# Performance work log

Measured on AMD Instinct MI355X. Metric: run time of the kernel, lower is better.

Reference implementation:

```python
import math
import jax, jax.numpy as jnp
import numpy as np

EMB = 1024
NHEADS = 16
CTX = 2048
LN_EPS = 1e-5


def new_gelu(x):
    c = math.sqrt(2.0 / math.pi)
    return 0.5 * x * (1.0 + jnp.tanh(c * (x + 0.044715 * x * x * x)))


def layer_norm(x, g, b):
    mu = jnp.mean(x, axis=-1, keepdims=True)
    var = jnp.mean(jnp.square(x - mu), axis=-1, keepdims=True)
    return (x - mu) * jax.lax.rsqrt(var + LN_EPS) * g + b


def setup_inputs() -> dict:
    key = jax.random.key(0)
    ks = jax.random.split(key, 12)
    s = 0.02
    return {
        "x": jax.random.normal(ks[0], (2, 2048, EMB), dtype=jnp.float32),
        "ln1_g": jnp.ones((EMB,), jnp.float32),
        "ln1_b": jnp.zeros((EMB,), jnp.float32),
        "W_attn": jax.random.normal(ks[1], (EMB, 3 * EMB), jnp.float32) * s,
        "b_attn": jnp.zeros((3 * EMB,), jnp.float32),
        "W_attn_proj": jax.random.normal(ks[2], (EMB, EMB), jnp.float32) * s,
        "b_attn_proj": jnp.zeros((EMB,), jnp.float32),
        "ln2_g": jnp.ones((EMB,), jnp.float32),
        "ln2_b": jnp.zeros((EMB,), jnp.float32),
        "W_fc": jax.random.normal(ks[3], (EMB, 4 * EMB), jnp.float32) * s,
        "b_fc": jnp.zeros((4 * EMB,), jnp.float32),
        "W_mlp_proj": jax.random.normal(ks[4], (4 * EMB, EMB), jnp.float32) * s,
        "b_mlp_proj": jnp.zeros((EMB,), jnp.float32),
    }


def reference(x, ln1_g, ln1_b, W_attn, b_attn, W_attn_proj, b_attn_proj,
              ln2_g, ln2_b, W_fc, b_fc, W_mlp_proj, b_mlp_proj):
    B, S, E = x.shape
    hd = E // NHEADS

    # x = ln_1(x)
    x = layer_norm(x, ln1_g, ln1_b)

    # attention on normalized x
    qkv = x @ W_attn + b_attn                      # [B,S,3E]
    q, k, v = jnp.split(qkv, 3, axis=-1)
    q = q.reshape(B, S, NHEADS, hd).transpose(0, 2, 1, 3)  # [B,H,S,hd]
    k = k.reshape(B, S, NHEADS, hd).transpose(0, 2, 1, 3)
    v = v.reshape(B, S, NHEADS, hd).transpose(0, 2, 1, 3)

    attn = jnp.einsum("bhqd,bhkd->bhqk", q, k) * (1.0 / math.sqrt(hd))
    causal = jnp.tril(jnp.ones((S, S), dtype=bool))
    attn = jnp.where(causal[None, None], attn, -jnp.inf)
    attn = jax.nn.softmax(attn, axis=-1)
    out = jnp.einsum("bhqk,bhkd->bhqd", attn, v)   # [B,H,S,hd]
    out = out.transpose(0, 2, 1, 3).reshape(B, S, E)
    out = out @ W_attn_proj + b_attn_proj

    x = x + out

    # x = ln_2(x)
    x = layer_norm(x, ln2_g, ln2_b)

    # MLP on normalized x
    h = new_gelu(x @ W_fc + b_fc)
    h = h @ W_mlp_proj + b_mlp_proj
    return x + h
```

## Files before the change

### kernel.cpp

```cpp
#include <hip/hip_runtime.h>
#include <cstdint>

typedef __attribute__((ext_vector_type(8))) short bf16x8;
typedef __attribute__((ext_vector_type(4))) float f32x4;
typedef __attribute__((ext_vector_type(4))) unsigned short u16x4;
typedef unsigned short u16;

#define LOG2E 1.44269504088896340736f

__device__ __forceinline__ u16 f2bf(float f) {
  unsigned u = __builtin_bit_cast(unsigned, f);
  u += 0x7FFFu + ((u >> 16) & 1u);
  return (u16)(u >> 16);
}
__device__ __forceinline__ float bf2f(u16 h) {
  return __builtin_bit_cast(float, ((unsigned)h) << 16);
}

#define GLOAD_LDS16(g, l)                                                              \
  __builtin_amdgcn_global_load_lds((const __attribute__((address_space(1))) void*)(g), \
                                   (__attribute__((address_space(3))) void*)(l), 16, 0, 0)

__global__ __launch_bounds__(256) void k_transpose_bf16(
    const float* __restrict__ W, u16* __restrict__ Wt, int K, int N) {
  __shared__ float tile[32][33];
  const int tid = threadIdx.x;
  const int tx = tid & 31, ty = tid >> 5;
  const int n0 = blockIdx.x * 32, k0 = blockIdx.y * 32;
#pragma unroll
  for (int i = 0; i < 32; i += 8)
    tile[ty + i][tx] = W[(size_t)(k0 + ty + i) * N + n0 + tx];
  __syncthreads();
#pragma unroll
  for (int i = 0; i < 32; i += 8)
    Wt[(size_t)(n0 + ty + i) * K + k0 + tx] = f2bf(tile[tx][ty + i]);
}

__global__ __launch_bounds__(256) void k_layernorm_bf16(
    const float* __restrict__ x, const float* __restrict__ g,
    const float* __restrict__ b, u16* __restrict__ y) {
  const int row = blockIdx.x, tid = threadIdx.x;
  const float4 v = ((const float4*)(x + (size_t)row * 1024))[tid];
  float s = v.x + v.y + v.z + v.w;
#pragma unroll
  for (int m = 1; m < 64; m <<= 1) s += __shfl_xor(s, m);
  __shared__ float ps[8];
  if ((tid & 63) == 0) ps[tid >> 6] = s;
  __syncthreads();
  const float mean = (ps[0] + ps[1] + ps[2] + ps[3]) * (1.0f / 1024.0f);
  const float d0 = v.x - mean, d1 = v.y - mean, d2 = v.z - mean, d3 = v.w - mean;
  float s2 = d0 * d0 + d1 * d1 + d2 * d2 + d3 * d3;
#pragma unroll
  for (int m = 1; m < 64; m <<= 1) s2 += __shfl_xor(s2, m);
  if ((tid & 63) == 0) ps[4 + (tid >> 6)] = s2;
  __syncthreads();
  const float var = (ps[4] + ps[5] + ps[6] + ps[7]) * (1.0f / 1024.0f);
  const float rstd = rsqrtf(var + 1e-5f);
  const float4 gv = ((const float4*)g)[tid];
  const float4 bv = ((const float4*)b)[tid];
  u16x4 o;
  o[0] = f2bf(d0 * rstd * gv.x + bv.x);
  o[1] = f2bf(d1 * rstd * gv.y + bv.y);
  o[2] = f2bf(d2 * rstd * gv.z + bv.z);
  o[3] = f2bf(d3 * rstd * gv.w + bv.w);
  *(u16x4*)(y + (size_t)row * 1024 + tid * 4) = o;
}

__device__ __forceinline__ float gelu_f(float x) {
  const float u = 0.7978845608028654f * (x + 0.044715f * x * x * x);
  const float e = exp2f(u * 2.8853900817779268f);
  const float t = 1.0f - 2.0f / (e + 1.0f);
  return 0.5f * x * (1.0f + t);
}

template <int EPI>
__global__ __launch_bounds__(256, 2) void k_gemm_bt(
    const u16* __restrict__ A, const u16* __restrict__ Bt,
    const float* __restrict__ bias, const u16* __restrict__ resid,
    void* __restrict__ out, u16* __restrict__ vt, int M, int N, int K) {
  __shared__ u16 As[2][128 * 64];
  __shared__ u16 Bs[2][128 * 64];
  const int tid = threadIdx.x;
  const int rowBase = blockIdx.y * 128, colBase = blockIdx.x * 128;
  const int w = tid >> 6, l = tid & 63;
  const int wm = w >> 1, wn = w & 1;
  const int lrow = l & 15, lg = l >> 4;
  const int srow = tid >> 3, sslot = tid & 7;

  const f32x4 fz = {0.f, 0.f, 0.f, 0.f};
  f32x4 acc[4][4];
#pragma unroll
  for (int m = 0; m < 4; m++)
#pragma unroll
    for (int n = 0; n < 4; n++) acc[m][n] = fz;

  const int NT = K >> 6;
  auto STAGE = [&](int b, int kt) {
#pragma unroll
    for (int i = 0; i < 4; i++) {
      const int r = srow + 32 * i;
      const int gs = sslot ^ (r & 7);
      GLOAD_LDS16(A + (size_t)(rowBase + r) * K + kt * 64 + gs * 8,
                  (char*)As[b] + i * 4096 + tid * 16);
      GLOAD_LDS16(Bt + (size_t)(colBase + r) * K + kt * 64 + gs * 8,
                  (char*)Bs[b] + i * 4096 + tid * 16);
    }
  };

  STAGE(0, 0);
  for (int kt = 0; kt < NT; ++kt) {
    const int buf = kt & 1;
    if (kt + 1 < NT) {
      STAGE(buf ^ 1, kt + 1);
      asm volatile("s_waitcnt vmcnt(8)" ::: "memory");
    } else {
      asm volatile("s_waitcnt vmcnt(0)" ::: "memory");
    }
    __builtin_amdgcn_s_barrier();
    const char* Ab = (const char*)As[buf];
    const char* Bb = (const char*)Bs[buf];
#pragma unroll
    for (int kc = 0; kc < 2; kc++) {
      bf16x8 av[4], bv[4];
#pragma unroll
      for (int m = 0; m < 4; m++) {
        const int r = wm * 64 + m * 16 + lrow;
        const int sl = (kc * 4 + lg) ^ (r & 7);
        av[m] = *(const bf16x8*)(Ab + r * 128 + sl * 16);
      }
#pragma unroll
      for (int n = 0; n < 4; n++) {
        const int r = wn * 64 + n * 16 + lrow;
        const int sl = (kc * 4 + lg) ^ (r & 7);
        bv[n] = *(const bf16x8*)(Bb + r * 128 + sl * 16);
      }
#pragma unroll
      for (int m = 0; m < 4; m++)
#pragma unroll
        for (int n = 0; n < 4; n++)
          acc[m][n] = __builtin_amdgcn_mfma_f32_16x16x32_bf16(av[m], bv[n], acc[m][n], 0, 0, 0);
    }
    __builtin_amdgcn_s_barrier();
  }
#pragma unroll
  for (int n = 0; n < 4; n++) {
    const int col = colBase + wn * 64 + n * 16 + lrow;
    const float bval = bias[col];
#pragma unroll
    for (int m = 0; m < 4; m++) {
      const int row0 = rowBase + wm * 64 + m * 16 + lg * 4;
      if (EPI == 3 && col >= 2048) {
        const int c2 = col - 2048;
        const int hh = c2 >> 6, dd = c2 & 63;
        const int bat = row0 >> 11, tok0 = row0 & 2047;
        u16x4 pk;
#pragma unroll
        for (int r = 0; r < 4; r++) pk[r] = f2bf(acc[m][n][r] + bval);
        *(u16x4*)(vt + ((size_t)(bat * 16 + hh) * 64 + dd) * 2048 + tok0) = pk;
      } else if (EPI == 3) {
#pragma unroll
        for (int r = 0; r < 4; r++)
          ((u16*)out)[(size_t)(row0 + r) * 2048 + col] = f2bf(acc[m][n][r] + bval);
      } else {
#pragma unroll
        for (int r = 0; r < 4; r++) {
          const size_t idx = (size_t)(row0 + r) * N + col;
          float v = acc[m][n][r] + bval;
          if (EPI == 0) {
            ((u16*)out)[idx] = f2bf(v);
          } else if (EPI == 2) {
            ((u16*)out)[idx] = f2bf(gelu_f(v));
          } else {
            v += bf2f(resid[idx]);
            ((float*)out)[idx] = v;
          }
        }
      }
    }
  }
}

__global__ __launch_bounds__(256, 4) void k_attention(
    const u16* __restrict__ qk, const u16* __restrict__ VT, u16* __restrict__ out) {
  const int S = 2048, E2 = 2048;
  const int bid = blockIdx.x;
  const int qt = 31 - (bid >> 5);
  const int bh = bid & 31;
  const int bat = bh >> 4, h = bh & 15;
  const u16* base = qk + (size_t)bat * S * E2;
  const u16* kbase = base + 1024 + h * 64;
  const u16* vbase = VT + (size_t)bh * 64 * S;
  const int tid = threadIdx.x, w = tid >> 6, l = tid & 63;
  const int lrow = l & 15, lg = l >> 4;
  __shared__ u16 Ks[2][64 * 64];
  __shared__ u16 Vs[2][64 * 64];
  __shared__ u16 Pl[4][16 * 64];
  u16* Plw = Pl[w];
  const int srow = tid >> 3, sslot = tid & 7;
  const int gs = sslot ^ (srow & 7);
  const float sc = 0.125f * LOG2E;
  const f32x4 fz = {0.f, 0.f, 0.f, 0.f};

  auto STAGE = [&](int bufi, int kb) {
#pragma unroll
    for (int round = 0; round < 2; round++) {
      const int r = srow + 32 * round;
      GLOAD_LDS16(kbase + (size_t)(kb + r) * E2 + gs * 8, (char*)Ks[bufi] + round * 4096 + tid * 16);
      GLOAD_LDS16(vbase + (size_t)r * S + kb + gs * 8, (char*)Vs[bufi] + round * 4096 + tid * 16);
    }
  };

  const int qrow0 = qt * 64 + w * 16;
  const int nkt = qt + 1;

  bf16x8 qfrag[2];
#pragma unroll
  for (int kc = 0; kc < 2; kc++)
    qfrag[kc] = *(const bf16x8*)(base + (size_t)(qrow0 + lrow) * E2 + h * 64 + kc * 32 + lg * 8);

  f32x4 o[4];
  float mrow[4], lsum[4];
#pragma unroll
  for (int r = 0; r < 4; r++) { mrow[r] = -1e30f; lsum[r] = 0.f; }
#pragma unroll
  for (int df = 0; df < 4; df++) o[df] = fz;

  STAGE(0, 0);
  __syncthreads();

  for (int kt = 0; kt < nkt; kt++) {
    const int cur = kt & 1;
    const int kb = kt * 64;
    if (kt + 1 < nkt) STAGE(cur ^ 1, kb + 64);
    const u16* Kc = Ks[cur];
    const u16* Vc = Vs[cur];

    f32x4 sv[4];
#pragma unroll
    for (int kf = 0; kf < 4; kf++) sv[kf] = fz;
#pragma unroll
    for (int kc = 0; kc < 2; kc++) {
      bf16x8 kfr[4];
#pragma unroll
      for (int kf = 0; kf < 4; kf++) {
        const int rk = kf * 16 + lrow;
        kfr[kf] = *(const bf16x8*)(Kc + rk * 64 + ((kc * 4 + lg) ^ (rk & 7)) * 8);
      }
#pragma unroll
      for (int kf = 0; kf < 4; kf++)
        sv[kf] = __builtin_amdgcn_mfma_f32_16x16x32_bf16(qfrag[kc], kfr[kf], sv[kf], 0, 0, 0);
    }
#pragma unroll
    for (int kf = 0; kf < 4; kf++)
#pragma unroll
      for (int r = 0; r < 4; r++) sv[kf][r] *= sc;
    if (kt == nkt - 1) {
#pragma unroll
      for (int kf = 0; kf < 4; kf++) {
        const int kg = kb + kf * 16 + lrow;
#pragma unroll
        for (int r = 0; r < 4; r++) {
          const int qg = qrow0 + lg * 4 + r;
          if (kg > qg) sv[kf][r] = -1e30f;
        }
      }
    }
#pragma unroll
    for (int r = 0; r < 4; r++) {
      float mx = fmaxf(fmaxf(sv[0][r], sv[1][r]), fmaxf(sv[2][r], sv[3][r]));
#pragma unroll
      for (int msk = 1; msk < 16; msk <<= 1) mx = fmaxf(mx, __shfl_xor(mx, msk));
      const float mnew = fmaxf(mrow[r], mx);
      const float corr = exp2f(mrow[r] - mnew);
      mrow[r] = mnew;
      lsum[r] *= corr;
#pragma unroll
      for (int df = 0; df < 4; df++) o[df][r] *= corr;
      float rsv = 0.f;
#pragma unroll
      for (int kf = 0; kf < 4; kf++) {
        const float p = exp2f(sv[kf][r] - mnew);
        sv[kf][r] = p;
        rsv += p;
      }
#pragma unroll
      for (int msk = 1; msk < 16; msk <<= 1) rsv += __shfl_xor(rsv, msk);
      lsum[r] += rsv;
    }
#pragma unroll
    for (int kf = 0; kf < 4; kf++)
#pragma unroll
      for (int r = 0; r < 4; r++) {
        const int q = lg * 4 + r;
        *(u16*)((char*)Plw + q * 128 + ((kf * 32 + lrow * 2) ^ ((q & 7) << 4))) = f2bf(sv[kf][r]);
      }
#pragma unroll
    for (int kc = 0; kc < 2; kc++) {
      const bf16x8 pa =
          *(const bf16x8*)((const char*)Plw + lrow * 128 + (((kc * 4 + lg) ^ (lrow & 7)) << 4));
      bf16x8 vb[4];
#pragma unroll
      for (int df = 0; df < 4; df++) {
        const int rd = df * 16 + lrow;
        vb[df] = *(const bf16x8*)(Vc + rd * 64 + ((kc * 4 + lg) ^ (rd & 7)) * 8);
      }
#pragma unroll
      for (int df = 0; df < 4; df++)
        o[df] = __builtin_amdgcn_mfma_f32_16x16x32_bf16(pa, vb[df], o[df], 0, 0, 0);
    }
    __syncthreads();
  }
#pragma unroll
  for (int r = 0; r < 4; r++) {
    const float inv = 1.0f / lsum[r];
    const int qg = qrow0 + lg * 4 + r;
#pragma unroll
    for (int df = 0; df < 4; df++) {
      const int col = h * 64 + df * 16 + lrow;
      out[(size_t)(bat * S + qg) * 1024 + col] = f2bf(o[df][r] * inv);
    }
  }
}

extern "C" void kernel_launch(void* const* d_in, const int* in_sizes, int n_in,
                              void* d_out, int out_size, void* d_ws, size_t ws_size,
                              hipStream_t stream) {
  (void)in_sizes; (void)n_in; (void)out_size; (void)ws_size;
  const float* x      = (const float*)d_in[0];
  const float* ln1_g  = (const float*)d_in[1];
  const float* ln1_b  = (const float*)d_in[2];
  const float* W_attn = (const float*)d_in[3];
  const float* b_attn = (const float*)d_in[4];
  const float* W_proj = (const float*)d_in[5];
  const float* b_proj = (const float*)d_in[6];
  const float* ln2_g  = (const float*)d_in[7];
  const float* ln2_b  = (const float*)d_in[8];
  const float* W_fc   = (const float*)d_in[9];
  const float* b_fc   = (const float*)d_in[10];
  const float* W_mlp  = (const float*)d_in[11];
  const float* b_mlp  = (const float*)d_in[12];

  const int M = 4096;
  char* ws = (char*)d_ws;
  size_t off = 0;
  auto alloc = [&](size_t bytes) {
    void* p = ws + off;
    off += (bytes + 255) & ~(size_t)255;
    return p;
  };
  u16* WattnT = (u16*)alloc((size_t)3072 * 1024 * 2);
  u16* WprojT = (u16*)alloc((size_t)1024 * 1024 * 2);
  u16* WfcT   = (u16*)alloc((size_t)4096 * 1024 * 2);
  u16* WmlpT  = (u16*)alloc((size_t)1024 * 4096 * 2);
  u16* x1     = (u16*)alloc((size_t)M * 1024 * 2);
  u16* qkb    = (u16*)alloc((size_t)M * 2048 * 2);
  u16* VT     = (u16*)alloc((size_t)32 * 64 * 2048 * 2);
  u16* attno  = (u16*)alloc((size_t)M * 1024 * 2);
  float* x2   = (float*)alloc((size_t)M * 1024 * 4);
  u16* x3     = (u16*)alloc((size_t)M * 1024 * 2);
  u16* hbuf   = (u16*)alloc((size_t)M * 4096 * 2);

  const dim3 blk(256);
  k_transpose_bf16<<<dim3(3072 / 32, 1024 / 32), blk, 0, stream>>>(W_attn, WattnT, 1024, 3072);
  k_transpose_bf16<<<dim3(1024 / 32, 1024 / 32), blk, 0, stream>>>(W_proj, WprojT, 1024, 1024);
  k_transpose_bf16<<<dim3(4096 / 32, 1024 / 32), blk, 0, stream>>>(W_fc, WfcT, 1024, 4096);
  k_transpose_bf16<<<dim3(1024 / 32, 4096 / 32), blk, 0, stream>>>(W_mlp, WmlpT, 4096, 1024);

  k_layernorm_bf16<<<M, blk, 0, stream>>>(x, ln1_g, ln1_b, x1);
  k_gemm_bt<3><<<dim3(3072 / 128, M / 128), blk, 0, stream>>>(
      x1, WattnT, b_attn, nullptr, qkb, VT, M, 3072, 1024);
  k_attention<<<dim3(1024), blk, 0, stream>>>(qkb, VT, attno);
  k_gemm_bt<1><<<dim3(1024 / 128, M / 128), blk, 0, stream>>>(
      attno, WprojT, b_proj, x1, x2, nullptr, M, 1024, 1024);
  k_layernorm_bf16<<<M, blk, 0, stream>>>(x2, ln2_g, ln2_b, x3);
  k_gemm_bt<2><<<dim3(4096 / 128, M / 128), blk, 0, stream>>>(
      x3, WfcT, b_fc, nullptr, hbuf, nullptr, M, 4096, 1024);
  k_gemm_bt<1><<<dim3(1024 / 128, M / 128), blk, 0, stream>>>(
      hbuf, WmlpT, b_mlp, x3, d_out, nullptr, M, 1024, 4096);
}
```

Before: 277.8 us.

## Rewrite attention with 32x32 MFMA, 128-row query tiles and register-resident P

The attention kernel now gives each block 128 query rows, with each wave owning 32 rows, and uses 32x32x16 bf16 MFMAs that compute the transposed score tile (K as A operand, Q as B operand). The softmax probabilities are packed with v_cvt_pk_bf16_f32 and exchanged across half-waves with shuffles, so P goes straight into the PV MFMA without an LDS round trip. The online-softmax rescale is skipped unless the row max grows beyond a fixed threshold, which avoids most correction multiplies. This halves the grid and the occupancy target, and waves whose diagonal tile has passed sit idle while the rest of the block finishes the remaining K tiles, which could hurt load balance.

```diff
diff --git a/kernel.cpp b/kernel.cpp
--- a/kernel.cpp
+++ b/kernel.cpp
@@ -3,7 +3,9 @@
 
 typedef __attribute__((ext_vector_type(8))) short bf16x8;
 typedef __attribute__((ext_vector_type(4))) float f32x4;
+typedef __attribute__((ext_vector_type(16))) float f32x16;
 typedef __attribute__((ext_vector_type(4))) unsigned short u16x4;
+typedef __attribute__((ext_vector_type(4))) unsigned int u32x4;
 typedef unsigned short u16;
 
 #define LOG2E 1.44269504088896340736f
@@ -180,26 +182,24 @@
   }
 }
 
-__global__ __launch_bounds__(256, 4) void k_attention(
+__global__ __launch_bounds__(256, 2) void k_attention(
     const u16* __restrict__ qk, const u16* __restrict__ VT, u16* __restrict__ out) {
   const int S = 2048, E2 = 2048;
   const int bid = blockIdx.x;
-  const int qt = 31 - (bid >> 5);
+  const int qt = 15 - (bid >> 5);
   const int bh = bid & 31;
   const int bat = bh >> 4, h = bh & 15;
   const u16* base = qk + (size_t)bat * S * E2;
   const u16* kbase = base + 1024 + h * 64;
   const u16* vbase = VT + (size_t)bh * 64 * S;
   const int tid = threadIdx.x, w = tid >> 6, l = tid & 63;
-  const int lrow = l & 15, lg = l >> 4;
+  const int l31 = l & 31, lh = l >> 5;
   __shared__ u16 Ks[2][64 * 64];
   __shared__ u16 Vs[2][64 * 64];
-  __shared__ u16 Pl[4][16 * 64];
-  u16* Plw = Pl[w];
-  const int srow = tid >> 3, sslot = tid & 7;
-  const int gs = sslot ^ (srow & 7);
+  const int srow = tid >> 3;
+  const int gs = (tid & 7) ^ (srow & 7);
   const float sc = 0.125f * LOG2E;
-  const f32x4 fz = {0.f, 0.f, 0.f, 0.f};
+  const float RTHR = 8.0f / sc;
 
   auto STAGE = [&](int bufi, int kb) {
 #pragma unroll
@@ -210,115 +210,131 @@
     }
   };
 
-  const int qrow0 = qt * 64 + w * 16;
-  const int nkt = qt + 1;
-
-  bf16x8 qfrag[2];
-#pragma unroll
-  for (int kc = 0; kc < 2; kc++)
-    qfrag[kc] = *(const bf16x8*)(base + (size_t)(qrow0 + lrow) * E2 + h * 64 + kc * 32 + lg * 8);
-
-  f32x4 o[4];
-  float mrow[4], lsum[4];
-#pragma unroll
-  for (int r = 0; r < 4; r++) { mrow[r] = -1e30f; lsum[r] = 0.f; }
-#pragma unroll
-  for (int df = 0; df < 4; df++) o[df] = fz;
+  const int wq0 = qt * 128 + w * 32;
+  const int qg = wq0 + l31;
+  const int tdiag = wq0 >> 6;
+  const int nkt = 2 * qt + 2;
+
+  bf16x8 qf[4];
+#pragma unroll
+  for (int s = 0; s < 4; s++)
+    qf[s] = *(const bf16x8*)(base + (size_t)qg * E2 + h * 64 + s * 16 + lh * 8);
+
+  f32x16 o0, o1;
+#pragma unroll
+  for (int r = 0; r < 16; r++) { o0[r] = 0.f; o1[r] = 0.f; }
+  float mrow = -1e30f, lsum = 0.f;
 
   STAGE(0, 0);
   __syncthreads();
 
-  for (int kt = 0; kt < nkt; kt++) {
-    const int cur = kt & 1;
-    const int kb = kt * 64;
-    if (kt + 1 < nkt) STAGE(cur ^ 1, kb + 64);
-    const u16* Kc = Ks[cur];
-    const u16* Vc = Vs[cur];
-
-    f32x4 sv[4];
-#pragma unroll
-    for (int kf = 0; kf < 4; kf++) sv[kf] = fz;
-#pragma unroll
-    for (int kc = 0; kc < 2; kc++) {
-      bf16x8 kfr[4];
-#pragma unroll
-      for (int kf = 0; kf < 4; kf++) {
-        const int rk = kf * 16 + lrow;
-        kfr[kf] = *(const bf16x8*)(Kc + rk * 64 + ((kc * 4 + lg) ^ (rk & 7)) * 8);
-      }
-#pragma unroll
-      for (int kf = 0; kf < 4; kf++)
-        sv[kf] = __builtin_amdgcn_mfma_f32_16x16x32_bf16(qfrag[kc], kfr[kf], sv[kf], 0, 0, 0);
-    }
-#pragma unroll
-    for (int kf = 0; kf < 4; kf++)
-#pragma unroll
-      for (int r = 0; r < 4; r++) sv[kf][r] *= sc;
-    if (kt == nkt - 1) {
-#pragma unroll
-      for (int kf = 0; kf < 4; kf++) {
-        const int kg = kb + kf * 16 + lrow;
-#pragma unroll
-        for (int r = 0; r < 4; r++) {
-          const int qg = qrow0 + lg * 4 + r;
-          if (kg > qg) sv[kf][r] = -1e30f;
+  for (int t = 0; t < nkt; t++) {
+    const int cur = t & 1;
+    const int kb = t * 64;
+    if (t + 1 < nkt) STAGE(cur ^ 1, kb + 64);
+    if (t <= tdiag) {
+      const u16* Kc = Ks[cur];
+      const u16* Vc = Vs[cur];
+
+      f32x16 sv0, sv1;
+#pragma unroll
+      for (int r = 0; r < 16; r++) { sv0[r] = 0.f; sv1[r] = 0.f; }
+#pragma unroll
+      for (int s = 0; s < 4; s++) {
+        const int row0 = l31, row1 = 32 + l31;
+        const int sl = s * 2 + lh;
+        const bf16x8 k0 = *(const bf16x8*)(Kc + row0 * 64 + ((sl ^ (row0 & 7)) * 8));
+        const bf16x8 k1 = *(const bf16x8*)(Kc + row1 * 64 + ((sl ^ (row1 & 7)) * 8));
+        sv0 = __builtin_amdgcn_mfma_f32_32x32x16_bf16(k0, qf[s], sv0, 0, 0, 0);
+        sv1 = __builtin_amdgcn_mfma_f32_32x32x16_bf16(k1, qf[s], sv1, 0, 0, 0);
+      }
+
+      if (t == tdiag) {
+#pragma unroll
+        for (int reg = 0; reg < 16; reg++) {
+          const int kl = (reg & 3) + 8 * (reg >> 2) + 4 * lh;
+          if (kb + kl > qg) sv0[reg] = -1e30f;
+          if (kb + 32 + kl > qg) sv1[reg] = -1e30f;
         }
       }
-    }
-#pragma unroll
-    for (int r = 0; r < 4; r++) {
-      float mx = fmaxf(fmaxf(sv[0][r], sv[1][r]), fmaxf(sv[2][r], sv[3][r]));
-#pragma unroll
-      for (int msk = 1; msk < 16; msk <<= 1) mx = fmaxf(mx, __shfl_xor(mx, msk));
-      const float mnew = fmaxf(mrow[r], mx);
-      const float corr = exp2f(mrow[r] - mnew);
-      mrow[r] = mnew;
-      lsum[r] *= corr;
-#pragma unroll
-      for (int df = 0; df < 4; df++) o[df][r] *= corr;
-      float rsv = 0.f;
-#pragma unroll
-      for (int kf = 0; kf < 4; kf++) {
-        const float p = exp2f(sv[kf][r] - mnew);
-        sv[kf][r] = p;
-        rsv += p;
-      }
-#pragma unroll
-      for (int msk = 1; msk < 16; msk <<= 1) rsv += __shfl_xor(rsv, msk);
-      lsum[r] += rsv;
-    }
-#pragma unroll
-    for (int kf = 0; kf < 4; kf++)
-#pragma unroll
-      for (int r = 0; r < 4; r++) {
-        const int q = lg * 4 + r;
-        *(u16*)((char*)Plw + q * 128 + ((kf * 32 + lrow * 2) ^ ((q & 7) << 4))) = f2bf(sv[kf][r]);
-      }
-#pragma unroll
-    for (int kc = 0; kc < 2; kc++) {
-      const bf16x8 pa =
-          *(const bf16x8*)((const char*)Plw + lrow * 128 + (((kc * 4 + lg) ^ (lrow & 7)) << 4));
-      bf16x8 vb[4];
-#pragma unroll
-      for (int df = 0; df < 4; df++) {
-        const int rd = df * 16 + lrow;
-        vb[df] = *(const bf16x8*)(Vc + rd * 64 + ((kc * 4 + lg) ^ (rd & 7)) * 8);
-      }
-#pragma unroll
-      for (int df = 0; df < 4; df++)
-        o[df] = __builtin_amdgcn_mfma_f32_16x16x32_bf16(pa, vb[df], o[df], 0, 0, 0);
+
+      float tmax = sv0[0];
+#pragma unroll
+      for (int reg = 1; reg < 16; reg++) tmax = fmaxf(tmax, sv0[reg]);
+#pragma unroll
+      for (int reg = 0; reg < 16; reg++) tmax = fmaxf(tmax, sv1[reg]);
+      tmax = fmaxf(tmax, __shfl_xor(tmax, 32));
+
+      if (!__all(tmax - mrow <= RTHR)) {
+        const float mnew = fmaxf(mrow, tmax);
+        const float corr = exp2f((mrow - mnew) * sc);
+        lsum *= corr;
+#pragma unroll
+        for (int reg = 0; reg < 16; reg++) { o0[reg] *= corr; o1[reg] *= corr; }
+        mrow = mnew;
+      }
+      const float msc = mrow * sc;
+
+      float p0[16], p1[16];
+      float rsum = 0.f;
+#pragma unroll
+      for (int reg = 0; reg < 16; reg++) {
+        p0[reg] = exp2f(fmaf(sv0[reg], sc, -msc));
+        p1[reg] = exp2f(fmaf(sv1[reg], sc, -msc));
+        rsum += p0[reg] + p1[reg];
+      }
+      rsum += __shfl_xor(rsum, 32);
+      lsum += rsum;
+
+      unsigned pk0[8], pk1[8], ex0[8], ex1[8];
+#pragma unroll
+      for (int j = 0; j < 8; j++) {
+        asm("v_cvt_pk_bf16_f32 %0, %1, %2" : "=v"(pk0[j]) : "v"(p0[2 * j]), "v"(p0[2 * j + 1]));
+        asm("v_cvt_pk_bf16_f32 %0, %1, %2" : "=v"(pk1[j]) : "v"(p1[2 * j]), "v"(p1[2 * j + 1]));
+        ex0[j] = (unsigned)__shfl_xor((int)pk0[j], 32);
+        ex1[j] = (unsigned)__shfl_xor((int)pk1[j], 32);
+      }
+      const bool lo = (lh == 0);
+
+#pragma unroll
+      for (int kh = 0; kh < 2; kh++) {
+#pragma unroll
+        for (int sl2 = 0; sl2 < 2; sl2++) {
+          const int ks = kh * 2 + sl2;
+          const unsigned* pk = kh ? pk1 : pk0;
+          const unsigned* ex = kh ? ex1 : ex0;
+          const int j0 = sl2 * 4;
+          const unsigned b0 = lo ? pk[j0 + 0] : ex[j0 + 2];
+          const unsigned b1 = lo ? pk[j0 + 1] : ex[j0 + 3];
+          const unsigned b2 = lo ? ex[j0 + 0] : pk[j0 + 2];
+          const unsigned b3 = lo ? ex[j0 + 1] : pk[j0 + 3];
+          const u32x4 pbu = {b0, b1, b2, b3};
+          const bf16x8 pb = __builtin_bit_cast(bf16x8, pbu);
+          const int sl = ks * 2 + lh;
+          const int r0 = l31, r1 = 32 + l31;
+          const bf16x8 v0 = *(const bf16x8*)(Vc + r0 * 64 + ((sl ^ (r0 & 7)) * 8));
+          const bf16x8 v1 = *(const bf16x8*)(Vc + r1 * 64 + ((sl ^ (r1 & 7)) * 8));
+          o0 = __builtin_amdgcn_mfma_f32_32x32x16_bf16(v0, pb, o0, 0, 0, 0);
+          o1 = __builtin_amdgcn_mfma_f32_32x32x16_bf16(v1, pb, o1, 0, 0, 0);
+        }
+      }
     }
     __syncthreads();
   }
-#pragma unroll
-  for (int r = 0; r < 4; r++) {
-    const float inv = 1.0f / lsum[r];
-    const int qg = qrow0 + lg * 4 + r;
-#pragma unroll
-    for (int df = 0; df < 4; df++) {
-      const int col = h * 64 + df * 16 + lrow;
-      out[(size_t)(bat * S + qg) * 1024 + col] = f2bf(o[df][r] * inv);
-    }
+
+  const float inv = 1.0f / lsum;
+  const size_t orow = (size_t)(bat * S + qg) * 1024 + h * 64;
+#pragma unroll
+  for (int g = 0; g < 4; g++) {
+    u16x4 s0, s1;
+#pragma unroll
+    for (int r = 0; r < 4; r++) {
+      s0[r] = f2bf(o0[4 * g + r] * inv);
+      s1[r] = f2bf(o1[4 * g + r] * inv);
+    }
+    const int d0 = 8 * g + 4 * lh;
+    *(u16x4*)(out + orow + d0) = s0;
+    *(u16x4*)(out + orow + 32 + d0) = s1;
   }
 }
 
@@ -369,7 +385,7 @@
   k_layernorm_bf16<<<M, blk, 0, stream>>>(x, ln1_g, ln1_b, x1);
   k_gemm_bt<3><<<dim3(3072 / 128, M / 128), blk, 0, stream>>>(
       x1, WattnT, b_attn, nullptr, qkb, VT, M, 3072, 1024);
-  k_attention<<<dim3(1024), blk, 0, stream>>>(qkb, VT, attno);
+  k_attention<<<dim3(512), blk, 0, stream>>>(qkb, VT, attno);
   k_gemm_bt<1><<<dim3(1024 / 128, M / 128), blk, 0, stream>>>(
       attno, WprojT, b_proj, x1, x2, nullptr, M, 1024, 1024);
   k_layernorm_bf16<<<M, blk, 0, stream>>>(x2, ln2_g, ln2_b, x3);
```

After: 266.4 us. 1.04x faster.
